# Kernel tuning notes

Hardware: AMD Instinct MI355X
Metric: run time of the kernel (lower is better)

## Reference

```python
import jax, jax.numpy as jnp
import numpy as np

B, L, DIM = 4, 2048, 512
H, D = 8, 64
SCALE = D ** -0.5
NEG = -10000.0


def setup_inputs() -> dict:
    key = jax.random.key(0)
    ks = jax.random.split(key, 5)
    std = 1.0 / np.sqrt(DIM)
    return {
        "x": jax.random.normal(ks[0], (B, L, DIM), dtype=jnp.float32),
        "wq": jax.random.normal(ks[1], (H * D, DIM), dtype=jnp.float32) * std,
        "wk": jax.random.normal(ks[2], (H * D, DIM), dtype=jnp.float32) * std,
        "wv": jax.random.normal(ks[3], (H * D, DIM), dtype=jnp.float32) * std,
        "wo": jax.random.normal(ks[4], (DIM, H * D), dtype=jnp.float32) * std,
    }


def reference(x, wq, wk, wv, wo):
    b, l, _ = x.shape
    # projections (torch Linear: y = x @ W.T), split heads -> [b,h,l,d]
    q = (x @ wq.T).reshape(b, l, H, D).transpose(0, 2, 1, 3)
    k = (x @ wk.T).reshape(b, l, H, D).transpose(0, 2, 1, 3)
    v = (x @ wv.T).reshape(b, l, H, D).transpose(0, 2, 1, 3)
    scores = jnp.einsum("bhld,bhsd->bhls", q, k) * SCALE
    scores = jnp.nan_to_num(scores, nan=0.0, posinf=10000.0, neginf=NEG)
    diag = jnp.eye(l, dtype=bool)[None, None]  # [1,1,l,l]
    scores = jnp.where(diag, NEG, scores)
    attn = jax.nn.softmax(scores, axis=-1)
    attn = jnp.where(diag, 0.0, attn)
    attn = jnp.nan_to_num(attn, nan=0.0, posinf=0.0, neginf=0.0)
    out = jnp.einsum("bhls,bhsd->bhld", attn, v)
    out = out.transpose(0, 2, 1, 3).reshape(b, l, H * D)
    return out @ wo.T
```

## Files before the change

### kernel.cpp

```cpp
#include <hip/hip_runtime.h>
#include <hip/hip_bf16.h>


#define Bsz 4
#define Lsz 2048
#define DIMsz 512
#define Hsz 8
#define Dsz 64

typedef _Float16 f16;
typedef __attribute__((ext_vector_type(8))) _Float16 f16x8;
typedef __attribute__((ext_vector_type(4))) _Float16 f16x4;
typedef __attribute__((ext_vector_type(2))) __fp16 fp16x2;
typedef __attribute__((ext_vector_type(4))) float f32x4;
typedef __attribute__((ext_vector_type(16))) float f32x16;
typedef unsigned int u32;
typedef __attribute__((ext_vector_type(2))) unsigned int u32x2;

#if __has_builtin(__builtin_amdgcn_exp2f)
#define EXP2(x) __builtin_amdgcn_exp2f(x)
#else
#define EXP2(x) __expf(0.6931471805599453f * (x))
#endif

__device__ __forceinline__ u32 pack2(float a, float b) {
#if __has_builtin(__builtin_amdgcn_cvt_pkrtz)
    fp16x2 h = __builtin_amdgcn_cvt_pkrtz(a, b);
    return __builtin_bit_cast(u32, h);
#else
    fp16x2 h; h.x = (__fp16)a; h.y = (__fp16)b;
    return __builtin_bit_cast(u32, h);
#endif
}

#if __has_builtin(__builtin_amdgcn_permlane32_swap)
__device__ __forceinline__ void plswap(u32& a, u32& b) {
    u32x2 r = __builtin_amdgcn_permlane32_swap(a, b, false, false);
    a = r.x; b = r.y;
}
#else
__device__ __forceinline__ void plswap(u32& a, u32& b) {
    u32 sa = (u32)__shfl_xor((int)a, 32);
    u32 sb = (u32)__shfl_xor((int)b, 32);
    bool hi = (threadIdx.x & 32) != 0;
    u32 na = hi ? sb : a;
    u32 nb = hi ? b : sa;
    a = na; b = nb;
}
#endif

__device__ __forceinline__ void gl2lds16(const void* g, void* l) {
    __builtin_amdgcn_global_load_lds(
        (const __attribute__((address_space(1))) u32*)g,
        (__attribute__((address_space(3))) u32*)l, 16, 0, 0);
}

__global__ __launch_bounds__(256) void pack_f16(
    const float* __restrict__ x, const float* __restrict__ wq,
    const float* __restrict__ wk, const float* __restrict__ wv,
    const float* __restrict__ wo,
    f16* __restrict__ xh, f16* __restrict__ w3h, f16* __restrict__ woh)
{
    int bx = blockIdx.x, seg, blk;
    if (bx < 4096) { seg = 0; blk = bx; }
    else { seg = 1 + ((bx - 4096) >> 8); blk = (bx - 4096) & 255; }
    const float* s; f16* d; float sc = 1.0f;
    switch (seg) {
        case 0: s = x;  d = xh;            break;
        case 1: s = wq; d = w3h;           sc = 0.18033688011112042f; break;
        case 2: s = wk; d = w3h + 262144;  break;
        case 3: s = wv; d = w3h + 524288;  break;
        default: s = wo; d = woh;          break;
    }
    int i = (blk * 256 + threadIdx.x) * 4;
    float4 v = *(const float4*)(s + i);
    f16x4 o;
    o.x = (f16)(v.x * sc); o.y = (f16)(v.y * sc);
    o.z = (f16)(v.z * sc); o.w = (f16)(v.w * sc);
    *(f16x4*)(d + i) = o;
}

__global__ __launch_bounds__(256) void gemm_qkv_f16(
    const f16* __restrict__ A, const f16* __restrict__ B,
    f16* __restrict__ qh, f16* __restrict__ kh, f16* __restrict__ vth)
{
    __shared__ __align__(16) char smem[32768];
    f16* Ash = (f16*)smem;
    f16* Bsh = (f16*)(smem + 16384);

    const int tid = threadIdx.x;
    const int w = tid >> 6, lane = tid & 63;
    const int quad = lane >> 4, low = lane & 15;
    const int wm = w >> 1, wn = w & 1;
    const int m0 = blockIdx.y * 128, n0 = blockIdx.x * 128;

    f32x4 acc[4][4];
    #pragma unroll
    for (int i = 0; i < 4; i++)
        #pragma unroll
        for (int j = 0; j < 4; j++) acc[i][j] = (f32x4){0.f, 0.f, 0.f, 0.f};

    #pragma unroll 1
    for (int k0 = 0; k0 < DIMsz; k0 += 64) {
        __syncthreads();
        #pragma unroll
        for (int j = 0; j < 4; j++) {
            int t = j * 256 + tid;
            int r = t >> 3, g = t & 7;
            int gc = (g ^ (r & 7)) * 8;
            char* lb = (char*)Ash + (j * 256 + w * 64) * 16;
            gl2lds16(A + (size_t)(m0 + r) * DIMsz + k0 + gc, lb);
            char* lb2 = (char*)Bsh + (j * 256 + w * 64) * 16;
            gl2lds16(B + (size_t)(n0 + r) * DIMsz + k0 + gc, lb2);
        }
        __syncthreads();

        #pragma unroll
        for (int ks2 = 0; ks2 < 2; ks2++) {
            f16x8 af[4], bf[4];
            #pragma unroll
            for (int mt = 0; mt < 4; mt++) {
                int ar = wm * 64 + mt * 16 + low;
                int c = ks2 * 4 + quad;
                af[mt] = *(const f16x8*)&Ash[ar * 64 + ((c ^ (ar & 7)) << 3)];
            }
            #pragma unroll
            for (int nt = 0; nt < 4; nt++) {
                int br = wn * 64 + nt * 16 + low;
                int c = ks2 * 4 + quad;
                bf[nt] = *(const f16x8*)&Bsh[br * 64 + ((c ^ (br & 7)) << 3)];
            }
            #pragma unroll
            for (int mt = 0; mt < 4; mt++)
                #pragma unroll
                for (int nt = 0; nt < 4; nt++)
                    acc[mt][nt] = __builtin_amdgcn_mfma_f32_16x16x32_f16(
                        af[mt], bf[nt], acc[mt][nt], 0, 0, 0);
        }
    }

    const int proj = n0 >> 9;
    if (proj < 2) {
        f16* dst = (proj == 0) ? qh : kh;
        #pragma unroll
        for (int nt = 0; nt < 4; nt++) {
            int n = n0 + wn * 64 + nt * 16 + low;
            int c = n & 511, h = c >> 6, d = c & 63;
            #pragma unroll
            for (int mt = 0; mt < 4; mt++)
                #pragma unroll
                for (int r = 0; r < 4; r++) {
                    int m = m0 + wm * 64 + mt * 16 + quad * 4 + r;
                    int b_ = m >> 11, l = m & (Lsz - 1);
                    size_t bh = (size_t)(b_ * Hsz + h);
                    dst[(bh * Lsz + l) * Dsz + d] = (f16)acc[mt][nt][r];
                }
        }
    } else {
        const int hb = (n0 & 511) >> 6;
        f16* Tv = (f16*)smem;
        const int b_ = m0 >> 11, l0 = m0 & (Lsz - 1);
        #pragma unroll 1
        for (int hs = 0; hs < 2; hs++) {
            __syncthreads();
            if (wn == hs) {
                #pragma unroll
                for (int nt = 0; nt < 4; nt++) {
                    int d = nt * 16 + low;
                    #pragma unroll
                    for (int mt = 0; mt < 4; mt++)
                        #pragma unroll
                        for (int r = 0; r < 4; r++) {
                            int l = wm * 64 + mt * 16 + quad * 4 + r;
                            Tv[d * 136 + l] = (f16)acc[mt][nt][r];
                        }
                }
            }
            __syncthreads();
            int d = tid >> 2, seg = tid & 3;
            size_t bh = (size_t)(b_ * Hsz + hb + hs);
            f16* dstp = vth + (bh * 64 + d) * (size_t)Lsz + l0 + seg * 32;
            const f16* srcp = Tv + d * 136 + seg * 32;
            #pragma unroll
            for (int j = 0; j < 4; j++)
                *(f16x8*)(dstp + j * 8) = *(const f16x8*)(srcp + j * 8);
        }
    }
}

__global__ __launch_bounds__(256, 3) void attn_mfma(
    const f16* __restrict__ q, const f16* __restrict__ k,
    const f16* __restrict__ vt, f16* __restrict__ ctx)
{
    __shared__ __align__(16) char smem[49664];

    const int tid = threadIdx.x;
    const int w = tid >> 6, lane = tid & 63;
    const int col = lane & 31;
    const int h = lane >> 5;
    const int kw = w & 1, qw = w >> 1;
    const int bh = blockIdx.x;
    const int qb = blockIdx.y;
    const int q0 = qb * 64;
    const size_t kvb = (size_t)bh * Lsz;

    f16* Ks = (f16*)smem;
    f16* Vs = (f16*)(smem + 24576);

    f16x8 qf[4];
    #pragma unroll
    for (int s = 0; s < 4; s++)
        qf[s] = *(const f16x8*)(q + (kvb + q0 + qw * 32 + col) * Dsz
                                  + s * 16 + h * 8);
    #pragma unroll
    for (int s = 0; s < 4; s++)
        asm volatile("" :: "v"(qf[s]));

    const f16* kp; const f16* vp;
    {
        int r8 = tid >> 3, g8 = tid & 7;
        int gc = (g8 ^ (r8 & 7) ^ ((r8 >> 3) & 3)) << 3;
        kp = k + (kvb + r8) * Dsz + gc;
        vp = vt + ((size_t)bh * Dsz + r8) * Lsz + gc;
    }
    char* kl = (char*)smem + w * 1024;
    char* vl = (char*)smem + 24576 + w * 1024;

    const int cswz = (col & 7) ^ ((col >> 3) & 3);
    const f16* kfp[4];
    #pragma unroll
    for (int s = 0; s < 4; s++)
        kfp[s] = Ks + (kw * 32 + col) * 64 + (((s * 2 + h) ^ cswz) << 3);
    const f16* vfp[2][2];
    #pragma unroll
    for (int dt = 0; dt < 2; dt++)
        #pragma unroll
        for (int ks = 0; ks < 2; ks++) {
            int cv = kw * 4 + ks * 2 + h;
            vfp[dt][ks] = Vs + (dt * 32 + col) * 64 + ((cv ^ cswz) << 3);
        }

    f32x16 acc[2];
    #pragma unroll
    for (int dt = 0; dt < 2; dt++)
        #pragma unroll
        for (int i = 0; i < 16; i++) acc[dt][i] = 0.f;
    float lsum = 0.f;

#if __has_builtin(__builtin_amdgcn_fdot2)
    fp16x2 one2; one2.x = (__fp16)1.0f; one2.y = (__fp16)1.0f;
#endif

    gl2lds16(kp,            kl);
    gl2lds16(kp + 32 * Dsz, kl + 4096);
    gl2lds16(vp,            vl);
    gl2lds16(vp + 32 * Lsz, vl + 4096);
    kp += 64 * Dsz;
    vp += 64;

    int off0 = 0, off1 = 8192, off2 = 16384;
    #pragma unroll 1
    for (int r = 0; r < Lsz / 64; ++r) {
        if (r < Lsz / 64 - 1) {
            gl2lds16(kp,            kl + off1);
            gl2lds16(kp + 32 * Dsz, kl + off1 + 4096);
            gl2lds16(vp,            vl + off1);
            gl2lds16(vp + 32 * Lsz, vl + off1 + 4096);
            kp += 64 * Dsz;
            vp += 64;
            asm volatile("s_waitcnt vmcnt(4)" ::: "memory");
        } else {
            asm volatile("s_waitcnt vmcnt(0)" ::: "memory");
        }
        __builtin_amdgcn_s_barrier();
        __builtin_amdgcn_sched_barrier(0);

        f32x16 st;
        #pragma unroll
        for (int i = 0; i < 16; i++) st[i] = 0.f;
        __builtin_amdgcn_s_setprio(1);
        #pragma unroll
        for (int s = 0; s < 4; s++) {
            f16x8 kf = *(const f16x8*)((const char*)kfp[s] + off0);
            st = __builtin_amdgcn_mfma_f32_32x32x16_f16(kf, qf[s], st, 0, 0, 0);
        }
        __builtin_amdgcn_s_setprio(0);

        #pragma unroll
        for (int i = 0; i < 16; i++) st[i] = EXP2(st[i]);
        if (r == qb && kw == qw) {
            #pragma unroll
            for (int i = 0; i < 16; i++) {
                int row = (i & 3) + 8 * (i >> 2) + 4 * h;
                st[i] = (row == col) ? 0.f : st[i];
            }
        }

        u32 P2[8];
        #pragma unroll
        for (int j = 0; j < 8; j++)
            P2[j] = pack2(st[2 * j], st[2 * j + 1]);

#if __has_builtin(__builtin_amdgcn_fdot2)
        #pragma unroll
        for (int j = 0; j < 8; j++)
            lsum = __builtin_amdgcn_fdot2(
                __builtin_bit_cast(fp16x2, P2[j]), one2, lsum, false);
#else
        #pragma unroll
        for (int i = 0; i < 16; i++) lsum += st[i];
#endif

        plswap(P2[0], P2[2]); plswap(P2[1], P2[3]);
        plswap(P2[4], P2[6]); plswap(P2[5], P2[7]);
        union { u32 u[4]; f16x8 v; } pfa, pfb;
        #pragma unroll
        for (int jj = 0; jj < 4; jj++) {
            pfa.u[jj] = P2[jj];
            pfb.u[jj] = P2[4 + jj];
        }

        __builtin_amdgcn_s_setprio(1);
        #pragma unroll
        for (int dt = 0; dt < 2; dt++) {
            f16x8 vf0 = *(const f16x8*)((const char*)vfp[dt][0] + off0);
            acc[dt] = __builtin_amdgcn_mfma_f32_32x32x16_f16(
                vf0, pfa.v, acc[dt], 0, 0, 0);
            f16x8 vf1 = *(const f16x8*)((const char*)vfp[dt][1] + off0);
            acc[dt] = __builtin_amdgcn_mfma_f32_32x32x16_f16(
                vf1, pfb.v, acc[dt], 0, 0, 0);
        }
        __builtin_amdgcn_s_setprio(0);

        int t_ = off0; off0 = off1; off1 = off2; off2 = t_;
    }

    __syncthreads();

    float* Lsp = (float*)(smem + 49152);
    lsum += __shfl_xor(lsum, 32);
    if (h == 0) Lsp[qw * 64 + kw * 32 + col] = lsum;

    float* Om = (float*)smem;
    if (kw == 1) {
        float* og = Om + qw * 2048;
        #pragma unroll
        for (int dt = 0; dt < 2; dt++)
            #pragma unroll
            for (int i = 0; i < 16; i++) {
                int row = (i & 3) + 8 * (i >> 2) + 4 * h;
                og[(dt * 32 + row) * 32 + col] = acc[dt][i];
            }
    }
    __syncthreads();
    if (kw == 0) {
        const float* og = Om + qw * 2048;
        #pragma unroll
        for (int dt = 0; dt < 2; dt++)
            #pragma unroll
            for (int i = 0; i < 16; i++) {
                int row = (i & 3) + 8 * (i >> 2) + 4 * h;
                acc[dt][i] += og[(dt * 32 + row) * 32 + col];
            }
        const int b = bh >> 3, hh = bh & 7;
        float ls = Lsp[qw * 64 + col] + Lsp[qw * 64 + 32 + col];
        const float inv = 1.0f / ls;
        f16* op = ctx + ((size_t)(b * Lsz + q0 + qw * 32 + col)) * DIMsz
                      + hh * 64;
        #pragma unroll
        for (int dt = 0; dt < 2; dt++)
            #pragma unroll
            for (int r4 = 0; r4 < 4; r4++) {
                f16x4 o;
                o.x = (f16)(acc[dt][4 * r4 + 0] * inv);
                o.y = (f16)(acc[dt][4 * r4 + 1] * inv);
                o.z = (f16)(acc[dt][4 * r4 + 2] * inv);
                o.w = (f16)(acc[dt][4 * r4 + 3] * inv);
                *(f16x4*)(op + dt * 32 + 8 * r4 + 4 * h) = o;
            }
    }
}

__global__ __launch_bounds__(256) void gemm_out_f16(
    const f16* __restrict__ A, const f16* __restrict__ B,
    float* __restrict__ C)
{
    __shared__ f16 Ash[64 * 64];
    __shared__ f16 Bsh[64 * 64];
    const int tid = threadIdx.x;
    const int w = tid >> 6, lane = tid & 63;
    const int quad = lane >> 4, low = lane & 15;
    const int wm = w >> 1, wn = w & 1;
    const int m0 = blockIdx.y * 64, n0 = blockIdx.x * 64;

    f32x4 acc[2][2];
    #pragma unroll
    for (int i = 0; i < 2; i++)
        #pragma unroll
        for (int j = 0; j < 2; j++) acc[i][j] = (f32x4){0.f, 0.f, 0.f, 0.f};

    #pragma unroll 1
    for (int k0 = 0; k0 < DIMsz; k0 += 64) {
        __syncthreads();
        #pragma unroll
        for (int j = 0; j < 2; j++) {
            int t = j * 256 + tid;
            int r = t >> 3, g = t & 7;
            int gc = (g ^ (r & 7)) * 8;
            char* lb = (char*)Ash + (j * 256 + w * 64) * 16;
            gl2lds16(A + (size_t)(m0 + r) * DIMsz + k0 + gc, lb);
            char* lb2 = (char*)Bsh + (j * 256 + w * 64) * 16;
            gl2lds16(B + (size_t)(n0 + r) * DIMsz + k0 + gc, lb2);
        }
        __syncthreads();

        #pragma unroll
        for (int ks2 = 0; ks2 < 2; ks2++) {
            f16x8 af[2], bf[2];
            #pragma unroll
            for (int mt = 0; mt < 2; mt++) {
                int ar = wm * 32 + mt * 16 + low;
                int c = ks2 * 4 + quad;
                af[mt] = *(const f16x8*)&Ash[ar * 64 + ((c ^ (ar & 7)) << 3)];
            }
            #pragma unroll
            for (int nt = 0; nt < 2; nt++) {
                int br = wn * 32 + nt * 16 + low;
                int c = ks2 * 4 + quad;
                bf[nt] = *(const f16x8*)&Bsh[br * 64 + ((c ^ (br & 7)) << 3)];
            }
            #pragma unroll
            for (int mt = 0; mt < 2; mt++)
                #pragma unroll
                for (int nt = 0; nt < 2; nt++)
                    acc[mt][nt] = __builtin_amdgcn_mfma_f32_16x16x32_f16(
                        af[mt], bf[nt], acc[mt][nt], 0, 0, 0);
        }
    }

    #pragma unroll
    for (int mt = 0; mt < 2; mt++)
        #pragma unroll
        for (int r = 0; r < 4; r++) {
            int m = m0 + wm * 32 + mt * 16 + quad * 4 + r;
            #pragma unroll
            for (int nt = 0; nt < 2; nt++) {
                int n = n0 + wn * 32 + nt * 16 + low;
                C[(size_t)m * DIMsz + n] = acc[mt][nt][r];
            }
        }
}

extern "C" void kernel_launch(void* const* d_in, const int* in_sizes, int n_in,
                              void* d_out, int out_size, void* d_ws, size_t ws_size,
                              hipStream_t stream) {
    const float* x  = (const float*)d_in[0];
    const float* wq = (const float*)d_in[1];
    const float* wk = (const float*)d_in[2];
    const float* wv = (const float*)d_in[3];
    const float* wo = (const float*)d_in[4];
    float* out = (float*)d_out;

    const size_t NTOK = (size_t)Bsz * Lsz;
    const size_t XSZ  = NTOK * DIMsz;

    f16* xh   = (f16*)d_ws;
    f16* w3h  = xh + XSZ;
    f16* woh  = w3h + 3 * 262144;
    f16* qh   = woh + 262144;
    f16* kh   = qh + XSZ;
    f16* vth  = kh + XSZ;
    f16* ctxh = vth + XSZ;

    pack_f16<<<5120, 256, 0, stream>>>(x, wq, wk, wv, wo, xh, w3h, woh);

    dim3 g1(1536 / 128, NTOK / 128);
    gemm_qkv_f16<<<g1, 256, 0, stream>>>(xh, w3h, qh, kh, vth);

    dim3 g2(Bsz * Hsz, Lsz / 64);
    attn_mfma<<<g2, 256, 0, stream>>>(qh, kh, vth, ctxh);

    dim3 g3(DIMsz / 64, NTOK / 64);
    gemm_out_f16<<<g3, 256, 0, stream>>>(ctxh, woh, out);
}
```

Measured before the change: 165.5 us.

## Deepen attention K/V prefetch to two stages and swizzle GEMM block order

After: 164.4 us. No clear change (-0.7%).

```diff
diff --git a/kernel.cpp b/kernel.cpp
--- a/kernel.cpp
+++ b/kernel.cpp
@@ -92,7 +92,9 @@
     const int w = tid >> 6, lane = tid & 63;
     const int quad = lane >> 4, low = lane & 15;
     const int wm = w >> 1, wn = w & 1;
-    const int m0 = blockIdx.y * 128, n0 = blockIdx.x * 128;
+    const int bid = blockIdx.x;
+    const int swz = (bid & 7) * 96 + (bid >> 3);
+    const int m0 = (swz / 12) * 128, n0 = (swz % 12) * 128;
 
     f32x4 acc[4][4];
     #pragma unroll
@@ -247,27 +249,29 @@
         for (int i = 0; i < 16; i++) acc[dt][i] = 0.f;
     float lsum = 0.f;
 
-#if __has_builtin(__builtin_amdgcn_fdot2)
-    fp16x2 one2; one2.x = (__fp16)1.0f; one2.y = (__fp16)1.0f;
-#endif
-
     gl2lds16(kp,            kl);
     gl2lds16(kp + 32 * Dsz, kl + 4096);
     gl2lds16(vp,            vl);
     gl2lds16(vp + 32 * Lsz, vl + 4096);
-    kp += 64 * Dsz;
-    vp += 64;
-
+    kp += 64 * Dsz; vp += 64;
+    gl2lds16(kp,            kl + 8192);
+    gl2lds16(kp + 32 * Dsz, kl + 8192 + 4096);
+    gl2lds16(vp,            vl + 8192);
+    gl2lds16(vp + 32 * Lsz, vl + 8192 + 4096);
+    kp += 64 * Dsz; vp += 64;
+
+    const int NR = Lsz / 64;
     int off0 = 0, off1 = 8192, off2 = 16384;
     #pragma unroll 1
-    for (int r = 0; r < Lsz / 64; ++r) {
-        if (r < Lsz / 64 - 1) {
-            gl2lds16(kp,            kl + off1);
-            gl2lds16(kp + 32 * Dsz, kl + off1 + 4096);
-            gl2lds16(vp,            vl + off1);
-            gl2lds16(vp + 32 * Lsz, vl + off1 + 4096);
-            kp += 64 * Dsz;
-            vp += 64;
+    for (int r = 0; r < NR; ++r) {
+        if (r < NR - 2) {
+            gl2lds16(kp,            kl + off2);
+            gl2lds16(kp + 32 * Dsz, kl + off2 + 4096);
+            gl2lds16(vp,            vl + off2);
+            gl2lds16(vp + 32 * Lsz, vl + off2 + 4096);
+            kp += 64 * Dsz; vp += 64;
+            asm volatile("s_waitcnt vmcnt(8)" ::: "memory");
+        } else if (r == NR - 2) {
             asm volatile("s_waitcnt vmcnt(4)" ::: "memory");
         } else {
             asm volatile("s_waitcnt vmcnt(0)" ::: "memory");
@@ -295,22 +299,13 @@
                 st[i] = (row == col) ? 0.f : st[i];
             }
         }
+        #pragma unroll
+        for (int i = 0; i < 16; i++) lsum += st[i];
 
         u32 P2[8];
         #pragma unroll
         for (int j = 0; j < 8; j++)
             P2[j] = pack2(st[2 * j], st[2 * j + 1]);
-
-#if __has_builtin(__builtin_amdgcn_fdot2)
-        #pragma unroll
-        for (int j = 0; j < 8; j++)
-            lsum = __builtin_amdgcn_fdot2(
-                __builtin_bit_cast(fp16x2, P2[j]), one2, lsum, false);
-#else
-        #pragma unroll
-        for (int i = 0; i < 16; i++) lsum += st[i];
-#endif
-
         plswap(P2[0], P2[2]); plswap(P2[1], P2[3]);
         plswap(P2[4], P2[6]); plswap(P2[5], P2[7]);
         union { u32 u[4]; f16x8 v; } pfa, pfb;
@@ -331,6 +326,8 @@
                 vf1, pfb.v, acc[dt], 0, 0, 0);
         }
         __builtin_amdgcn_s_setprio(0);
+        __builtin_amdgcn_sched_barrier(0);
+        __builtin_amdgcn_s_barrier();
 
         int t_ = off0; off0 = off1; off1 = off2; off2 = t_;
     }
@@ -391,7 +388,9 @@
     const int w = tid >> 6, lane = tid & 63;
     const int quad = lane >> 4, low = lane & 15;
     const int wm = w >> 1, wn = w & 1;
-    const int m0 = blockIdx.y * 64, n0 = blockIdx.x * 64;
+    const int bid = blockIdx.x;
+    const int swz = (bid & 7) * 128 + (bid >> 3);
+    const int m0 = (swz >> 3) * 64, n0 = (swz & 7) * 64;
 
     f32x4 acc[2][2];
     #pragma unroll
@@ -474,12 +473,10 @@
 
     pack_f16<<<5120, 256, 0, stream>>>(x, wq, wk, wv, wo, xh, w3h, woh);
 
-    dim3 g1(1536 / 128, NTOK / 128);
-    gemm_qkv_f16<<<g1, 256, 0, stream>>>(xh, w3h, qh, kh, vth);
+    gemm_qkv_f16<<<768, 256, 0, stream>>>(xh, w3h, qh, kh, vth);
 
     dim3 g2(Bsz * Hsz, Lsz / 64);
     attn_mfma<<<g2, 256, 0, stream>>>(qh, kh, vth, ctxh);
 
-    dim3 g3(DIMsz / 64, NTOK / 64);
-    gemm_out_f16<<<g3, 256, 0, stream>>>(ctxh, woh, out);
-}
+    gemm_out_f16<<<1024, 256, 0, stream>>>(ctxh, woh, out);
+}
```
